# Performance work log

Hardware: AMD Instinct MI355X
Metric: run time of the kernel (lower is better)

The kernel has to match this reference:

```python
import jax, jax.numpy as jnp
import numpy as np

# J2 (von Mises) plane-strain elastoplasticity with linear isotropic hardening
# (faithful stand-in for pyprnn's J2Material: elastic predictor + radial return,
#  committed history = plastic strain tensor + accumulated plastic strain).
E_MOD = 3130.0   # Young's modulus (epoxy, MPa)
NU = 0.37        # Poisson ratio
SIG_Y = 64.8     # initial yield stress
H_ISO = 300.0    # linear isotropic hardening modulus
MU = E_MOD / (2.0 * (1.0 + NU))
LAM = E_MOD * NU / ((1.0 + NU) * (1.0 - 2.0 * NU))


def j2_update(eps, eps_p, alpha):
    """eps: [P,3] (exx, eyy, gamma_xy engineering); eps_p: [P,4] (xx,yy,zz,xy tensorial);
    alpha: [P] accumulated plastic strain. Returns (stress [P,3], eps_p_new, alpha_new)."""
    ee_xx = eps[:, 0] - eps_p[:, 0]
    ee_yy = eps[:, 1] - eps_p[:, 1]
    ee_zz = -eps_p[:, 2]                      # plane strain: total ezz = 0
    ee_xy = 0.5 * eps[:, 2] - eps_p[:, 3]     # tensorial shear
    tr = ee_xx + ee_yy + ee_zz
    # trial (elastic predictor) stress
    sxx = LAM * tr + 2.0 * MU * ee_xx
    syy = LAM * tr + 2.0 * MU * ee_yy
    szz = LAM * tr + 2.0 * MU * ee_zz
    sxy = 2.0 * MU * ee_xy
    p = (sxx + syy + szz) / 3.0
    dxx, dyy, dzz = sxx - p, syy - p, szz - p
    q = jnp.sqrt(1.5 * (dxx * dxx + dyy * dyy + dzz * dzz + 2.0 * sxy * sxy))
    f = q - (SIG_Y + H_ISO * alpha)
    dgam = jnp.maximum(f, 0.0) / (3.0 * MU + H_ISO)   # radial return, closed form
    qs = jnp.maximum(q, 1e-12)
    nxx, nyy, nzz, nxy = 1.5 * dxx / qs, 1.5 * dyy / qs, 1.5 * dzz / qs, 1.5 * sxy / qs
    two_mu_dg = 2.0 * MU * dgam
    sig = jnp.stack([sxx - two_mu_dg * nxx, syy - two_mu_dg * nyy, sxy - two_mu_dg * nxy], axis=-1)
    eps_p_new = eps_p + dgam[:, None] * jnp.stack([nxx, nyy, nzz, nxy], axis=-1)
    alpha_new = alpha + dgam
    return sig, eps_p_new, alpha_new


def setup_inputs() -> dict:
    key = jax.random.key(0)
    k1, k2, k3 = jax.random.split(key, 3)
    B, T, F = 16384, 128, 3
    MATPTS = 16
    L, O = MATPTS * F, 3
    x = jax.random.normal(k1, (B, T, F), dtype=jnp.float32) * 0.02  # strain paths
    W1 = jax.random.normal(k2, (L, F), dtype=jnp.float32) * (1.0 / np.sqrt(F))
    W2 = jax.random.normal(k3, (O, L), dtype=jnp.float32) * (1.0 / np.sqrt(L))
    return {"x": x, "W1": W1, "W2": W2}


def reference(x, W1, W2):
    B, T, F = x.shape
    L = W1.shape[0]
    P = B * (L // F)                 # total material points = batch * mat_pts
    W2s = jax.nn.softplus(W2)        # SoftLayer: positive weights, no bias
    xt = jnp.swapaxes(x, 0, 1)       # [T, B, F]

    def step(carry, xi):
        eps_p, alpha = carry
        lat = xi @ W1.T                       # fc1 (no bias): [B, L]
        eps = lat.reshape(P, F)               # per-material-point strain
        sig, eps_p, alpha = j2_update(eps, eps_p, alpha)   # update + commit
        out = sig.reshape(B, L) @ W2s.T       # fc2 softplus-weighted linear
        return (eps_p, alpha), out

    carry0 = (jnp.zeros((P, 4), jnp.float32), jnp.zeros((P,), jnp.float32))
    _, ys = jax.lax.scan(step, carry0, xt)    # ys: [T, B, O]
    return jnp.swapaxes(ys, 0, 1)             # [B, T, O]
```

## Files before the change

kernel.cpp:

```cpp
#include <hip/hip_runtime.h>
#include <math.h>


#define BLOCK 128
#define BPB 16
#define TSTEPS 128
#define ROWF (TSTEPS * 3)

typedef float v2 __attribute__((ext_vector_type(2)));

static __device__ __forceinline__ v2 vfma(v2 a, v2 b, v2 c) {
    return __builtin_elementwise_fma(a, b, c);
}
static __device__ __forceinline__ v2 vmax(v2 a, v2 b) {
    return __builtin_elementwise_max(a, b);
}

#define DPP_ADDST(v, ctrl)                                                   \
    v += __int_as_float(__builtin_amdgcn_update_dpp(                         \
        0, __float_as_int(v), (ctrl), 0xf, 0xf, true))
#define RED8(v)                                                              \
    do { DPP_ADDST(v, 0xB1); DPP_ADDST(v, 0x4E); DPP_ADDST(v, 0x141); } while (0)

#define DPP_ST(r, ctrl) "v_add_f32_dpp %" #r ", %" #r ", %" #r " " ctrl \
                        " row_mask:0xf bank_mask:0xf\n\t"
#define DPP_STAGE24(ctrl) \
    DPP_ST(0, ctrl)  DPP_ST(1, ctrl)  DPP_ST(2, ctrl)  DPP_ST(3, ctrl)  \
    DPP_ST(4, ctrl)  DPP_ST(5, ctrl)  DPP_ST(6, ctrl)  DPP_ST(7, ctrl)  \
    DPP_ST(8, ctrl)  DPP_ST(9, ctrl)  DPP_ST(10, ctrl) DPP_ST(11, ctrl) \
    DPP_ST(12, ctrl) DPP_ST(13, ctrl) DPP_ST(14, ctrl) DPP_ST(15, ctrl) \
    DPP_ST(16, ctrl) DPP_ST(17, ctrl) DPP_ST(18, ctrl) DPP_ST(19, ctrl) \
    DPP_ST(20, ctrl) DPP_ST(21, ctrl) DPP_ST(22, ctrl) DPP_ST(23, ctrl)
#define DPP_BFLY24(a0,a1,a2,a3,a4,a5,a6,a7,a8,a9,a10,a11,                    \
                   a12,a13,a14,a15,a16,a17,a18,a19,a20,a21,a22,a23)          \
  asm volatile(                                                              \
    "s_nop 1\n\t"                                                            \
    DPP_STAGE24("quad_perm:[1,0,3,2]")                                       \
    DPP_STAGE24("quad_perm:[2,3,0,1]")                                       \
    DPP_STAGE24("row_half_mirror")                                           \
    : "+v"(a0), "+v"(a1), "+v"(a2), "+v"(a3), "+v"(a4), "+v"(a5),            \
      "+v"(a6), "+v"(a7), "+v"(a8), "+v"(a9), "+v"(a10), "+v"(a11),          \
      "+v"(a12), "+v"(a13), "+v"(a14), "+v"(a15), "+v"(a16), "+v"(a17),      \
      "+v"(a18), "+v"(a19), "+v"(a20), "+v"(a21), "+v"(a22), "+v"(a23))

__global__ __launch_bounds__(BLOCK, 2)
void prnn_j2_kernel(const float* __restrict__ x,
                    const float* __restrict__ W1,
                    const float* __restrict__ W2,
                    float* __restrict__ out)
{
    constexpr float MU    = (float)(3130.0 / (2.0 * (1.0 + 0.37)));
    constexpr float LAM   = (float)(3130.0 * 0.37 / ((1.0 + 0.37) * (1.0 - 2.0 * 0.37)));
    constexpr float SIG_Y = 64.8f;
    constexpr float H_ISO = 300.0f;
    const float TWO_MU  = 2.0f * MU;
    const float INV_DEN = 1.0f / (3.0f * MU + H_ISO);
    const float K3P     = (3.0f * MU) * INV_DEN;
    const float HP      = H_ISO * INV_DEN;
    const float CSC     = 1.0f / (MU * 2.4494897427831781f);
    const float Y0      = SIG_Y * CSC;
    const float SQRT2   = 1.41421356237309515f;
    const float RSQRT2  = 0.70710678118654752f;

    const int tid = threadIdx.x;
    const int g   = tid >> 3;
    const int l   = tid & 7;
    const int gb  = blockIdx.x * BPB + g;

    const float* xb = x + gb * ROWF;
    float* ob = out + gb * ROWF;

    const int pa = l, pb = l + 8;
    v2 w1r0[3], w1r1[3], w1h2[3];
    #pragma unroll
    for (int f = 0; f < 3; ++f) {
        w1r0[f].x = W1[(3 * pa + 0) * 3 + f];
        w1r0[f].y = W1[(3 * pb + 0) * 3 + f];
        w1r1[f].x = W1[(3 * pa + 1) * 3 + f];
        w1r1[f].y = W1[(3 * pb + 1) * 3 + f];
        w1h2[f].x = 0.5f * W1[(3 * pa + 2) * 3 + f];
        w1h2[f].y = 0.5f * W1[(3 * pb + 2) * 3 + f];
    }
    v2 w2p[3][3];
    #pragma unroll
    for (int o = 0; o < 3; ++o)
        #pragma unroll
        for (int c = 0; c < 3; ++c) {
            float wa = W2[o * 48 + 3 * pa + c];
            float wb = W2[o * 48 + 3 * pb + c];
            w2p[o][c].x = fmaxf(wa, 0.0f) + log1pf(expf(-fabsf(wa)));
            w2p[o][c].y = fmaxf(wb, 0.0f) + log1pf(expf(-fabsf(wb)));
        }

    float Mrow[3];
    {
        float Ms[3][3];
        #pragma unroll
        for (int f = 0; f < 3; ++f) {
            v2 ax = (LAM + TWO_MU) * w1r0[f] + LAM * w1r1[f];
            v2 ay = LAM * w1r0[f] + (LAM + TWO_MU) * w1r1[f];
            v2 as = TWO_MU * w1h2[f];
            #pragma unroll
            for (int o = 0; o < 3; ++o) {
                v2 mp = vfma(w2p[o][0], ax, vfma(w2p[o][1], ay, w2p[o][2] * as));
                float ms = mp.x + mp.y;
                RED8(ms);
                Ms[o][f] = ms;
            }
        }
        #pragma unroll
        for (int f = 0; f < 3; ++f) {
            float v = (l == 0) ? Ms[0][f] : ((l == 1) ? Ms[1][f] : Ms[2][f]);
            Mrow[f] = v;
        }
    }

    v2 wdx[3], wdy[3], wsh[3];
    #pragma unroll
    for (int f = 0; f < 3; ++f) {
        wdx[f] = (2.0f * w1r0[f] - w1r1[f]) * (1.0f / 3.0f);
        wdy[f] = (2.0f * w1r1[f] - w1r0[f]) * (1.0f / 3.0f);
        wsh[f] = SQRT2 * w1h2[f];
    }
    #pragma unroll
    for (int o = 0; o < 3; ++o) w2p[o][2] *= RSQRT2;

    v2 p0 = {0.f,0.f}, p1 = {0.f,0.f}, ps = {0.f,0.f};
    v2 Y  = {Y0, Y0};
    v2 z0 = {0.f,0.f}, z1 = {0.f,0.f}, z2 = {0.f,0.f};

    const float4* xv = (const float4*)xb;
    const bool wact = (l < 3);
    float* obl = ob + l;

#define J2_PHYS(x0_, x1_, x2_, rr, mxv)                                      \
  {                                                                          \
    const float x0s = (x0_), x1s = (x1_), x2s = (x2_);                       \
    const v2 x0 = {x0s, x0s}, x1 = {x1s, x1s}, x2 = {x2s, x2s};              \
    const v2 ex0 = vfma(wdx[0], x0, vfma(wdx[1], x1, wdx[2] * x2));          \
    const v2 ey0 = vfma(wdy[0], x0, vfma(wdy[1], x1, wdy[2] * x2));          \
    const v2 wsy = vfma(wsh[0], x0, vfma(wsh[1], x1, wsh[2] * x2));          \
    const v2 exd = ex0 - p0;                                                 \
    const v2 eyd = ey0 - p1;                                                 \
    const v2 exy = wsy - ps;                                                 \
    const v2 szd = exd + eyd;                             \
    const v2 ua = vfma(eyd, eyd, vfma(exd, exd, (v2){1e-30f, 1e-30f}));      \
    const v2 ub = vfma(exy, exy, szd * szd);                                 \
    const v2 u = ua + ub;                      \
    v2 rq;                                                                   \
    rq.x = __builtin_amdgcn_rsqf(u.x);                                       \
    rq.y = __builtin_amdgcn_rsqf(u.y);                                       \
    const v2 gm = vmax(vfma(-Y, rq, (v2){1.0f, 1.0f}), (v2){0.0f, 0.0f});    \
    const v2 su = u * rq;                    \
    const v2 k  = K3P * gm;                                                  \
    Y = vfma((v2){HP, HP}, gm * su, Y);        \
    const v2 kdx = k * exd;                                                  \
    const v2 kdy = k * eyd;                                                  \
    const v2 kdp = k * exy;                                                  \
    p0 += kdx;                                                               \
    p1 += kdy;                                                               \
    ps += kdp;                                                               \
    z0 = vfma(w2p[0][0], kdx, vfma(w2p[0][1], kdy, vfma(w2p[0][2], kdp, z0)));\
    z1 = vfma(w2p[1][0], kdx, vfma(w2p[1][1], kdy, vfma(w2p[1][2], kdp, z1)));\
    z2 = vfma(w2p[2][0], kdx, vfma(w2p[2][1], kdy, vfma(w2p[2][2], kdp, z2)));\
    (rr)[0] = z0.x + z0.y;                                                   \
    (rr)[1] = z1.x + z1.y;                                                   \
    (rr)[2] = z2.x + z2.y;                                                   \
    (mxv) = fmaf(Mrow[0], x0s, fmaf(Mrow[1], x1s, Mrow[2] * x2s));           \
  }

    float4 A0 = xv[0], A1 = xv[1], A2 = xv[2];
    float4 A3 = xv[3], A4 = xv[4], A5 = xv[5];

    for (int tb = 0; tb < TSTEPS / 8; ++tb) {
        const int nb = (tb < TSTEPS / 8 - 1) ? (6 * tb + 6) : (6 * tb);
        float4 An0 = xv[nb + 0];
        float4 An1 = xv[nb + 1];
        float4 An2 = xv[nb + 2];
        float4 An3 = xv[nb + 3];
        float4 An4 = xv[nb + 4];
        float4 An5 = xv[nb + 5];

        float r[24], mx[8];
        J2_PHYS(A0.x, A0.y, A0.z, r + 0,  mx[0]);
        J2_PHYS(A0.w, A1.x, A1.y, r + 3,  mx[1]);
        J2_PHYS(A1.z, A1.w, A2.x, r + 6,  mx[2]);
        J2_PHYS(A2.y, A2.z, A2.w, r + 9,  mx[3]);
        J2_PHYS(A3.x, A3.y, A3.z, r + 12, mx[4]);
        J2_PHYS(A3.w, A4.x, A4.y, r + 15, mx[5]);
        J2_PHYS(A4.z, A4.w, A5.x, r + 18, mx[6]);
        J2_PHYS(A5.y, A5.z, A5.w, r + 21, mx[7]);

        DPP_BFLY24(r[0],  r[1],  r[2],  r[3],  r[4],  r[5],
                   r[6],  r[7],  r[8],  r[9],  r[10], r[11],
                   r[12], r[13], r[14], r[15], r[16], r[17],
                   r[18], r[19], r[20], r[21], r[22], r[23]);

        if (wact) {
            #pragma unroll
            for (int s = 0; s < 8; ++s) {
                float zz = (l == 0) ? r[3*s] : ((l == 1) ? r[3*s+1] : r[3*s+2]);
                obl[24 * tb + 3 * s] = fmaf(-TWO_MU, zz, mx[s]);
            }
        }

        A0 = An0; A1 = An1; A2 = An2;
        A3 = An3; A4 = An4; A5 = An5;
    }
#undef J2_PHYS
}

extern "C" void kernel_launch(void* const* d_in, const int* in_sizes, int n_in,
                              void* d_out, int out_size, void* d_ws, size_t ws_size,
                              hipStream_t stream) {
    const float* x  = (const float*)d_in[0];
    const float* W1 = (const float*)d_in[1];
    const float* W2 = (const float*)d_in[2];
    float* out = (float*)d_out;

    const int B = 16384;
    dim3 grid(B / BPB);
    dim3 block(BLOCK);
    prnn_j2_kernel<<<grid, block, 0, stream>>>(x, W1, W2, out);
}
```

Before: 114.8 us.

## Reformulate J2 state in fc2-projected coordinates to drop separate output accumulation

```diff
diff --git a/kernel.cpp b/kernel.cpp
--- a/kernel.cpp
+++ b/kernel.cpp
@@ -125,9 +125,46 @@
     #pragma unroll
     for (int o = 0; o < 3; ++o) w2p[o][2] *= RSQRT2;
 
-    v2 p0 = {0.f,0.f}, p1 = {0.f,0.f}, ps = {0.f,0.f};
+    v2 V[3][3];
+    #pragma unroll
+    for (int o = 0; o < 3; ++o)
+        #pragma unroll
+        for (int f = 0; f < 3; ++f)
+            V[o][f] = vfma(w2p[o][0], wdx[f],
+                      vfma(w2p[o][1], wdy[f], w2p[o][2] * wsh[f]));
+
+    v2 G00, G11, G22, TG01, TG02, TG12;
+    {
+        v2 A[3][3];
+        const v2 c00 = w2p[1][1]*w2p[2][2] - w2p[1][2]*w2p[2][1];
+        const v2 c01 = w2p[1][0]*w2p[2][2] - w2p[1][2]*w2p[2][0];
+        const v2 c02 = w2p[1][0]*w2p[2][1] - w2p[1][1]*w2p[2][0];
+        const v2 det = w2p[0][0]*c00 - w2p[0][1]*c01 + w2p[0][2]*c02;
+        const v2 rd  = (v2){1.0f, 1.0f} / det;
+        A[0][0] =  c00 * rd;
+        A[0][1] = (w2p[0][2]*w2p[2][1] - w2p[0][1]*w2p[2][2]) * rd;
+        A[0][2] = (w2p[0][1]*w2p[1][2] - w2p[0][2]*w2p[1][1]) * rd;
+        A[1][0] = -c01 * rd;
+        A[1][1] = (w2p[0][0]*w2p[2][2] - w2p[0][2]*w2p[2][0]) * rd;
+        A[1][2] = (w2p[0][2]*w2p[1][0] - w2p[0][0]*w2p[1][2]) * rd;
+        A[2][0] =  c02 * rd;
+        A[2][1] = (w2p[0][1]*w2p[2][0] - w2p[0][0]*w2p[2][1]) * rd;
+        A[2][2] = (w2p[0][0]*w2p[1][1] - w2p[0][1]*w2p[1][0]) * rd;
+        #define GFORM(i, j)                                                  \
+            (2.0f*(A[0][i]*A[0][j] + A[1][i]*A[1][j])                        \
+             + (A[0][i]*A[1][j] + A[1][i]*A[0][j])                           \
+             + A[2][i]*A[2][j])
+        G00 = GFORM(0, 0);
+        G11 = GFORM(1, 1);
+        G22 = GFORM(2, 2);
+        TG01 = 2.0f * GFORM(0, 1);
+        TG02 = 2.0f * GFORM(0, 2);
+        TG12 = 2.0f * GFORM(1, 2);
+        #undef GFORM
+    }
+
+    v2 q0 = {0.f,0.f}, q1 = {0.f,0.f}, q2 = {0.f,0.f};
     v2 Y  = {Y0, Y0};
-    v2 z0 = {0.f,0.f}, z1 = {0.f,0.f}, z2 = {0.f,0.f};
 
     const float4* xv = (const float4*)xb;
     const bool wact = (l < 3);
@@ -137,16 +174,17 @@
   {                                                                          \
     const float x0s = (x0_), x1s = (x1_), x2s = (x2_);                       \
     const v2 x0 = {x0s, x0s}, x1 = {x1s, x1s}, x2 = {x2s, x2s};              \
-    const v2 ex0 = vfma(wdx[0], x0, vfma(wdx[1], x1, wdx[2] * x2));          \
-    const v2 ey0 = vfma(wdy[0], x0, vfma(wdy[1], x1, wdy[2] * x2));          \
-    const v2 wsy = vfma(wsh[0], x0, vfma(wsh[1], x1, wsh[2] * x2));          \
-    const v2 exd = ex0 - p0;                                                 \
-    const v2 eyd = ey0 - p1;                                                 \
-    const v2 exy = wsy - ps;                                                 \
-    const v2 szd = exd + eyd;                             \
-    const v2 ua = vfma(eyd, eyd, vfma(exd, exd, (v2){1e-30f, 1e-30f}));      \
-    const v2 ub = vfma(exy, exy, szd * szd);                                 \
-    const v2 u = ua + ub;                      \
+    const v2 e0 = vfma(V[0][0], x0, vfma(V[0][1], x1, V[0][2] * x2));        \
+    const v2 e1 = vfma(V[1][0], x0, vfma(V[1][1], x1, V[1][2] * x2));        \
+    const v2 e2 = vfma(V[2][0], x0, vfma(V[2][1], x1, V[2][2] * x2));        \
+    const v2 a = e0 - q0;                                                    \
+    const v2 b = e1 - q1;                                                    \
+    const v2 c = e2 - q2;                                                    \
+    const v2 h0 = vfma(G00, a, vfma(TG01, b, TG02 * c));                     \
+    const v2 h1 = vfma(G11, b, TG12 * c);                                    \
+    const v2 cc = c * c;                                                     \
+    v2 u = vfma(h0, a, vfma(h1, b, G22 * cc));                               \
+    u = vmax(u, (v2){1e-30f, 1e-30f});       \
     v2 rq;                                                                   \
     rq.x = __builtin_amdgcn_rsqf(u.x);                                       \
     rq.y = __builtin_amdgcn_rsqf(u.y);                                       \
@@ -154,18 +192,12 @@
     const v2 su = u * rq;                    \
     const v2 k  = K3P * gm;                                                  \
     Y = vfma((v2){HP, HP}, gm * su, Y);        \
-    const v2 kdx = k * exd;                                                  \
-    const v2 kdy = k * eyd;                                                  \
-    const v2 kdp = k * exy;                                                  \
-    p0 += kdx;                                                               \
-    p1 += kdy;                                                               \
-    ps += kdp;                                                               \
-    z0 = vfma(w2p[0][0], kdx, vfma(w2p[0][1], kdy, vfma(w2p[0][2], kdp, z0)));\
-    z1 = vfma(w2p[1][0], kdx, vfma(w2p[1][1], kdy, vfma(w2p[1][2], kdp, z1)));\
-    z2 = vfma(w2p[2][0], kdx, vfma(w2p[2][1], kdy, vfma(w2p[2][2], kdp, z2)));\
-    (rr)[0] = z0.x + z0.y;                                                   \
-    (rr)[1] = z1.x + z1.y;                                                   \
-    (rr)[2] = z2.x + z2.y;                                                   \
+    q0 = vfma(k, a, q0);                                                     \
+    q1 = vfma(k, b, q1);                                                     \
+    q2 = vfma(k, c, q2);                                                     \
+    (rr)[0] = q0.x + q0.y;                                                   \
+    (rr)[1] = q1.x + q1.y;                                                   \
+    (rr)[2] = q2.x + q2.y;                                                   \
     (mxv) = fmaf(Mrow[0], x0s, fmaf(Mrow[1], x1s, Mrow[2] * x2s));           \
   }
 
```

Measured after the change: 113.1 us. About the same (-1.5%).
